# Optimization experiments

Measured on AMD Instinct MI355X. Metric: run time of the kernel, lower is better.

## Reference

```python
import jax, jax.numpy as jnp
import numpy as np

N_NODES = 25000
N_EDGES = 400000
IN = 128
HID = [64, 64, 128]
HEADS = [4, 4, 1]
SLOPE = 0.01  # F.leaky_relu default


def _xavier(key, shape):
    fan_out, fan_in = shape
    std = (2.0 / (fan_in + fan_out)) ** 0.5
    return std * jax.random.normal(key, shape, dtype=jnp.float32)


def setup_inputs() -> dict:
    key = jax.random.key(0)
    ks = jax.random.split(key, 24)
    inp = {}
    inp['x'] = jax.random.normal(ks[0], (N_NODES, IN), dtype=jnp.float32)
    inp['edge_weight'] = jax.random.uniform(ks[1], (N_EDGES,), dtype=jnp.float32)
    inp['edge_src'] = jax.random.randint(ks[2], (N_EDGES,), 0, N_NODES)
    inp['edge_dst'] = jax.random.randint(ks[3], (N_EDGES,), 0, N_NODES)
    inp['pos_src'] = jax.random.randint(ks[4], (100000,), 0, N_NODES)
    inp['pos_dst'] = jax.random.randint(ks[5], (100000,), 0, N_NODES)
    inp['neg_src'] = jax.random.randint(ks[6], (100000,), 0, N_NODES)
    inp['neg_dst'] = jax.random.randint(ks[7], (100000,), 0, N_NODES)
    # GAT layer params: fc weight [H*F, in], attn vector [F], bias [H*F]
    dims_in = [IN, HID[0] * HEADS[0], HID[1] * HEADS[1]]
    for l in range(3):
        H, F = HEADS[l], HID[l]
        inp[f'W{l}'] = _xavier(ks[8 + 2 * l], (H * F, dims_in[l]))
        inp[f'a{l}'] = _xavier(ks[9 + 2 * l], (1, F)).reshape(F)
        inp[f'b{l}'] = jnp.zeros((H * F,), dtype=jnp.float32)
    # predictor MLP: 128 -> 64 -> 32 -> 1 (Linear with bias)
    d = HID[2]
    inp['pW1'] = _xavier(ks[14], (d // 2, d)); inp['pb1'] = jnp.zeros((d // 2,), jnp.float32)
    inp['pW2'] = _xavier(ks[15], (d // 4, d // 2)); inp['pb2'] = jnp.zeros((d // 4,), jnp.float32)
    inp['pW3'] = _xavier(ks[16], (1, d // 4)); inp['pb3'] = jnp.zeros((1,), jnp.float32)
    return inp


def _leaky(x, slope=SLOPE):
    return jnp.where(x >= 0, x, slope * x)


def _gat_layer(x, W, a, b, src, dst, ew, H, F):
    N = x.shape[0]
    h = (x @ W.T).reshape(N, H, F)               # [N,H,F]
    hs = h[src]                                   # [E,H,F] gathered src feats
    # GATv2-style score: attn_fc(q_src + k_dst) per head
    score = jnp.einsum('ehf,f->eh', hs + h[dst], a)   # [E,H]
    e = _leaky(score + jnp.log1p(ew)[:, None])         # [E,H]
    # segment softmax over edges grouped by destination node
    m = jax.ops.segment_max(e, dst, num_segments=N)    # [N,H]
    m = jnp.where(jnp.isfinite(m), m, 0.0)             # guard empty segments
    ex = jnp.exp(e - m[dst])
    s = jax.ops.segment_sum(ex, dst, num_segments=N)   # [N,H]
    alpha = ex / jnp.maximum(s[dst], 1e-20)            # [E,H]
    out = jax.ops.segment_sum(alpha[:, :, None] * hs, dst, num_segments=N)  # [N,H,F]
    return out.reshape(N, H * F) + b


def _predictor(z, pW1, pb1, pW2, pb2, pW3, pb3):
    z = _leaky(z @ pW1.T + pb1, 0.2)
    z = _leaky(z @ pW2.T + pb2, 0.2)
    return z @ pW3.T + pb3


def reference(x, edge_weight, W0, a0, b0, W1, a1, b1, W2, a2, b2,
              pW1, pb1, pW2, pb2, pW3, pb3,
              edge_src, edge_dst, pos_src, pos_dst, neg_src, neg_dst):
    h = _gat_layer(x, W0, a0, b0, edge_src, edge_dst, edge_weight, HEADS[0], HID[0])
    h = _leaky(h)
    h = _gat_layer(h, W1, a1, b1, edge_src, edge_dst, edge_weight, HEADS[1], HID[1])
    h = _leaky(h)
    h = _gat_layer(h, W2, a2, b2, edge_src, edge_dst, edge_weight, HEADS[2], HID[2])
    gat_embedding = h
    h_pos = _predictor(h[pos_src] * h[pos_dst], pW1, pb1, pW2, pb2, pW3, pb3)
    h_neg = _predictor(h[neg_src] * h[neg_dst], pW1, pb1, pW2, pb2, pW3, pb3)
    return (h_pos, h_neg, gat_embedding)
```

## Files before the change

### kernel.cpp

```cpp
#include <hip/hip_runtime.h>
#include <math.h>

#define N_IN 128

__device__ __forceinline__ float leaky01(float x) { return x >= 0.f ? x : 0.01f * x; }
__device__ __forceinline__ float leaky02(float x) { return x >= 0.f ? x : 0.2f * x; }

__global__ void k_count(const int* __restrict__ edst, int* __restrict__ deg, int E) {
    int e = blockIdx.x * 256 + threadIdx.x;
    if (e < E) atomicAdd(&deg[edst[e]], 1);
}

__global__ void k_scan1(const int* __restrict__ deg, int* __restrict__ rowptr,
                        int* __restrict__ bsum, int n) {
    __shared__ int s[256];
    int b = blockIdx.x, t = threadIdx.x;
    int idx = b * 256 + t;
    int v = (idx < n) ? deg[idx] : 0;
    s[t] = v;
    __syncthreads();
    for (int off = 1; off < 256; off <<= 1) {
        int x = (t >= off) ? s[t - off] : 0;
        __syncthreads();
        s[t] += x;
        __syncthreads();
    }
    if (idx < n) rowptr[idx + 1] = s[t];
    if (t == 255) bsum[b] = s[255];
}

__global__ void k_scan2(const int* __restrict__ bsum, int* __restrict__ boff, int nb) {
    __shared__ int s[128];
    int t = threadIdx.x;
    int v = (t < nb) ? bsum[t] : 0;
    s[t] = v;
    __syncthreads();
    for (int off = 1; off < 128; off <<= 1) {
        int x = (t >= off) ? s[t - off] : 0;
        __syncthreads();
        s[t] += x;
        __syncthreads();
    }
    if (t < nb) boff[t] = s[t] - v;
}

__global__ void k_scan3(int* __restrict__ rowptr, const int* __restrict__ boff, int n) {
    int idx = blockIdx.x * 256 + threadIdx.x;
    if (idx < n) rowptr[idx + 1] += boff[idx >> 8];
    if (idx == 0) rowptr[0] = 0;
}

__global__ void k_fill(const int* __restrict__ esrc, const int* __restrict__ edst,
                       const float* __restrict__ ew, const int* __restrict__ rowptr,
                       int* __restrict__ cursor, int* __restrict__ eid,
                       int* __restrict__ csrc, float* __restrict__ clew, int E) {
    int e = blockIdx.x * 256 + threadIdx.x;
    if (e >= E) return;
    int d = edst[e];
    int slot = rowptr[d] + atomicAdd(&cursor[d], 1);
    eid[slot] = e;
    csrc[slot] = esrc[e];
    clew[slot] = log1pf(ew[e]);
}

__global__ void k_sortseg(const int* __restrict__ rowptr, int* __restrict__ eid,
                          int* __restrict__ csrc, float* __restrict__ clew, int n) {
    int v = blockIdx.x * 256 + threadIdx.x;
    if (v >= n) return;
    int b = rowptr[v], e = rowptr[v + 1];
    for (int i = b + 1; i < e; i++) {
        int ke = eid[i], ks = csrc[i];
        float kl = clew[i];
        int j = i - 1;
        while (j >= b && eid[j] > ke) {
            eid[j + 1] = eid[j]; csrc[j + 1] = csrc[j]; clew[j + 1] = clew[j];
            j--;
        }
        eid[j + 1] = ke; csrc[j + 1] = ks; clew[j + 1] = kl;
    }
}

__global__ __launch_bounds__(256) void k_gemm(const float* __restrict__ X,
                                              const float* __restrict__ W,
                                              float* __restrict__ C,
                                              int N, int K, int M,
                                              const float* __restrict__ avec,
                                              float* __restrict__ qaOut,
                                              int H, int F) {
    __shared__ float Xs[8][132];
    __shared__ float Ws[8][132];
    __shared__ float qred[128][17];
    int r0 = blockIdx.y * 128;
    int c0 = blockIdx.x * 128;
    int t = threadIdx.x;
    int ty = t >> 4, tx = t & 15;

    float acc[8][8];
#pragma unroll
    for (int i = 0; i < 8; i++)
#pragma unroll
        for (int j = 0; j < 8; j++) acc[i][j] = 0.f;

    int lr = t >> 1;
    int lk = (t & 1) * 4;
    bool xok = (r0 + lr) < N;
    const float* Xp = X + (size_t)(r0 + lr) * K + lk;
    const float* Wp = W + (size_t)(c0 + lr) * K + lk;

    for (int k0 = 0; k0 < K; k0 += 8) {
        float4 xv = xok ? *(const float4*)(Xp + k0) : make_float4(0.f, 0.f, 0.f, 0.f);
        float4 wv = *(const float4*)(Wp + k0);
        __syncthreads();
        Xs[lk + 0][lr] = xv.x; Xs[lk + 1][lr] = xv.y; Xs[lk + 2][lr] = xv.z; Xs[lk + 3][lr] = xv.w;
        Ws[lk + 0][lr] = wv.x; Ws[lk + 1][lr] = wv.y; Ws[lk + 2][lr] = wv.z; Ws[lk + 3][lr] = wv.w;
        __syncthreads();
#pragma unroll
        for (int k = 0; k < 8; k++) {
            float4 a0 = *(const float4*)&Xs[k][ty * 8];
            float4 a1 = *(const float4*)&Xs[k][ty * 8 + 4];
            float4 b0 = *(const float4*)&Ws[k][tx * 8];
            float4 b1 = *(const float4*)&Ws[k][tx * 8 + 4];
            float av[8] = {a0.x, a0.y, a0.z, a0.w, a1.x, a1.y, a1.z, a1.w};
            float bv[8] = {b0.x, b0.y, b0.z, b0.w, b1.x, b1.y, b1.z, b1.w};
#pragma unroll
            for (int i = 0; i < 8; i++)
#pragma unroll
                for (int j = 0; j < 8; j++) acc[i][j] += av[i] * bv[j];
        }
    }

#pragma unroll
    for (int i = 0; i < 8; i++) {
        int row = r0 + ty * 8 + i;
        if (row < N) {
            float4 v0 = make_float4(acc[i][0], acc[i][1], acc[i][2], acc[i][3]);
            float4 v1 = make_float4(acc[i][4], acc[i][5], acc[i][6], acc[i][7]);
            *(float4*)&C[(size_t)row * M + c0 + tx * 8] = v0;
            *(float4*)&C[(size_t)row * M + c0 + tx * 8 + 4] = v1;
        }
    }

    if (qaOut) {
        int f0 = (c0 + tx * 8) & (F - 1);
        float4 a0 = *(const float4*)&avec[f0];
        float4 a1 = *(const float4*)&avec[f0 + 4];
#pragma unroll
        for (int i = 0; i < 8; i++) {
            float s = acc[i][0] * a0.x + acc[i][1] * a0.y + acc[i][2] * a0.z + acc[i][3] * a0.w
                    + acc[i][4] * a1.x + acc[i][5] * a1.y + acc[i][6] * a1.z + acc[i][7] * a1.w;
            qred[ty * 8 + i][tx] = s;
        }
        __syncthreads();
        if (t < 128) {
            int R = r0 + t;
            if (R < N) {
                float s0 = 0.f, s1 = 0.f;
#pragma unroll
                for (int x = 0; x < 8; x++) { s0 += qred[t][x]; s1 += qred[t][x + 8]; }
                if (F == 64) {
                    int hb = c0 >> 6;
                    qaOut[(size_t)R * H + hb] = s0;
                    qaOut[(size_t)R * H + hb + 1] = s1;
                } else {
                    qaOut[R] = s0 + s1;
                }
            }
        }
    }
}

template <int H>
__global__ __launch_bounds__(256) void k_stats(const float* __restrict__ qa,
                                               const int* __restrict__ rowptr,
                                               const int* __restrict__ csr_src,
                                               const float* __restrict__ csr_lew,
                                               float* __restrict__ alf, int N) {
    int w = threadIdx.x >> 6;
    int l = threadIdx.x & 63;
    int n = blockIdx.x * 4 + w;
    if (n >= N) return;
    int beg = rowptr[n], end = rowptr[n + 1];
    if (beg >= end) return;

    float qd[H];
#pragma unroll
    for (int h = 0; h < H; h++) qd[h] = qa[(size_t)n * H + h];

    float mx[H];
#pragma unroll
    for (int h = 0; h < H; h++) mx[h] = -1e30f;
    for (int i = beg + l; i < end; i += 64) {
        int src = csr_src[i];
        float lw = csr_lew[i];
#pragma unroll
        for (int h = 0; h < H; h++) {
            float sc = leaky01(qa[(size_t)src * H + h] + qd[h] + lw);
            mx[h] = fmaxf(mx[h], sc);
        }
    }
#pragma unroll
    for (int h = 0; h < H; h++) {
        for (int off = 32; off > 0; off >>= 1)
            mx[h] = fmaxf(mx[h], __shfl_xor(mx[h], off, 64));
    }

    float sm[H];
#pragma unroll
    for (int h = 0; h < H; h++) sm[h] = 0.f;
    for (int i = beg + l; i < end; i += 64) {
        int src = csr_src[i];
        float lw = csr_lew[i];
#pragma unroll
        for (int h = 0; h < H; h++) {
            float sc = leaky01(qa[(size_t)src * H + h] + qd[h] + lw);
            sm[h] += __expf(sc - mx[h]);
        }
    }
#pragma unroll
    for (int h = 0; h < H; h++) {
        for (int off = 32; off > 0; off >>= 1)
            sm[h] += __shfl_xor(sm[h], off, 64);
    }
    float inv[H];
#pragma unroll
    for (int h = 0; h < H; h++) inv[h] = 1.f / fmaxf(sm[h], 1e-20f);

    for (int i = beg + l; i < end; i += 64) {
        int src = csr_src[i];
        float lw = csr_lew[i];
        float av[H];
#pragma unroll
        for (int h = 0; h < H; h++) {
            float sc = leaky01(qa[(size_t)src * H + h] + qd[h] + lw);
            av[h] = __expf(sc - mx[h]) * inv[h];
        }
        if (H == 4) {
            *(float4*)&alf[(size_t)i * 4] = make_float4(av[0], av[1], av[2], av[3]);
        } else {
            alf[i] = av[0];
        }
    }
}

template <int H, int F, int VW, bool LOUT>
__global__ __launch_bounds__(256) void k_aggv(const float* __restrict__ feat,
                                              const float* __restrict__ alf,
                                              const float* __restrict__ bias,
                                              const int* __restrict__ rowptr,
                                              const int* __restrict__ csr_src,
                                              float* __restrict__ out, int N) {
    constexpr int M = H * F;
    __shared__ int sh_src[4][64];
    __shared__ float sh_alpha[4][64 * H];
    int w = threadIdx.x >> 6, l = threadIdx.x & 63;
    int n = blockIdx.x * 4 + w;
    if (n >= N) return;
    int beg = rowptr[n];
    int deg = rowptr[n + 1] - beg;
    int c = l * VW;
    const int hh = c / F;

    float acc[VW];
#pragma unroll
    for (int j = 0; j < VW; j++) acc[j] = 0.f;

    for (int c0 = 0; c0 < deg; c0 += 64) {
        int cn = min(64, deg - c0);
        if (l < cn) {
            sh_src[w][l] = csr_src[beg + c0 + l];
            if (H == 4)
                *(float4*)&sh_alpha[w][l * 4] = *(const float4*)&alf[(size_t)(beg + c0 + l) * 4];
            else
                sh_alpha[w][l] = alf[beg + c0 + l];
        }
        int i = 0;
        for (; i + 2 <= cn; i += 2) {
            int s0 = sh_src[w][i], s1 = sh_src[w][i + 1];
            float a0 = sh_alpha[w][i * H + hh], a1 = sh_alpha[w][(i + 1) * H + hh];
            float f0[VW], f1[VW];
            if (VW == 4) {
                float4 v0 = *(const float4*)&feat[(size_t)s0 * M + c];
                float4 v1 = *(const float4*)&feat[(size_t)s1 * M + c];
                f0[0] = v0.x; f0[1] = v0.y; f0[2] = v0.z; f0[3] = v0.w;
                f1[0] = v1.x; f1[1] = v1.y; f1[2] = v1.z; f1[3] = v1.w;
            } else {
                float2 v0 = *(const float2*)&feat[(size_t)s0 * M + c];
                float2 v1 = *(const float2*)&feat[(size_t)s1 * M + c];
                f0[0] = v0.x; f0[1] = v0.y;
                f1[0] = v1.x; f1[1] = v1.y;
            }
#pragma unroll
            for (int j = 0; j < VW; j++) acc[j] += a0 * f0[j] + a1 * f1[j];
        }
        if (i < cn) {
            int s0 = sh_src[w][i];
            float a0 = sh_alpha[w][i * H + hh];
            float f0[VW];
            if (VW == 4) {
                float4 v0 = *(const float4*)&feat[(size_t)s0 * M + c];
                f0[0] = v0.x; f0[1] = v0.y; f0[2] = v0.z; f0[3] = v0.w;
            } else {
                float2 v0 = *(const float2*)&feat[(size_t)s0 * M + c];
                f0[0] = v0.x; f0[1] = v0.y;
            }
#pragma unroll
            for (int j = 0; j < VW; j++) acc[j] += a0 * f0[j];
        }
    }

#pragma unroll
    for (int j = 0; j < VW; j++) {
        float r = acc[j] + bias[c + j];
        if (LOUT) r = leaky01(r);
        out[(size_t)n * M + c + j] = r;
    }
}

__global__ __launch_bounds__(256) void k_predf6(const float* __restrict__ h2,
                                                const int* __restrict__ ps, const int* __restrict__ pd,
                                                const int* __restrict__ ns, const int* __restrict__ nd,
                                                const float* __restrict__ W1, const float* __restrict__ b1,
                                                const float* __restrict__ W2, const float* __restrict__ b2,
                                                const float* __restrict__ W3, const float* __restrict__ b3,
                                                float* __restrict__ out, int npos, int ntot) {
    __shared__ float Zs[128 * 36];
    __shared__ float Wc[32 * 68];
    __shared__ int sp[128], dp[128];

    int t = threadIdx.x;
    int p0 = blockIdx.x * 128;
    int ty2 = t >> 3;
    int tx2 = t & 7;

    if (t < 128) {
        int pr = p0 + t;
        int s = 0, d = 0;
        if (pr < ntot) {
            if (pr < npos) { s = ps[pr]; d = pd[pr]; }
            else           { s = ns[pr - npos]; d = nd[pr - npos]; }
        }
        sp[t] = s; dp[t] = d;
    }
    __syncthreads();

    float acc[4][8];
#pragma unroll
    for (int i = 0; i < 4; i++)
#pragma unroll
        for (int j = 0; j < 8; j++) acc[i][j] = 0.f;

    int sr = t >> 3;
    int sq = t & 7;

    for (int kc = 0; kc < 128; kc += 32) {
#pragma unroll
        for (int it = 0; it < 4; ++it) {
            int r = it * 32 + sr;
            int s = sp[r], d = dp[r];
            float4 a = *(const float4*)&h2[(size_t)s * 128 + kc + sq * 4];
            float4 b = *(const float4*)&h2[(size_t)d * 128 + kc + sq * 4];
            *(float4*)&Zs[r * 36 + sq * 4] =
                make_float4(a.x * b.x, a.y * b.y, a.z * b.z, a.w * b.w);
        }
        {
            int out_ = t & 63;
            int kh = (t >> 6) * 8;
            const float* wr = W1 + (size_t)out_ * 128 + kc + kh;
#pragma unroll
            for (int c = 0; c < 2; c++) {
                float4 wv = *(const float4*)(wr + c * 4);
                Wc[(kh + c * 4 + 0) * 68 + out_] = wv.x;
                Wc[(kh + c * 4 + 1) * 68 + out_] = wv.y;
                Wc[(kh + c * 4 + 2) * 68 + out_] = wv.z;
                Wc[(kh + c * 4 + 3) * 68 + out_] = wv.w;
            }
        }
        __syncthreads();
#pragma unroll
        for (int k4 = 0; k4 < 8; ++k4) {
            float4 a4[4];
#pragma unroll
            for (int i = 0; i < 4; i++)
                a4[i] = *(const float4*)&Zs[(ty2 + 32 * i) * 36 + k4 * 4];
#pragma unroll
            for (int kk = 0; kk < 4; ++kk) {
                float4 bA = *(const float4*)&Wc[(k4 * 4 + kk) * 68 + tx2 * 8];
                float4 bB = *(const float4*)&Wc[(k4 * 4 + kk) * 68 + tx2 * 8 + 4];
                float bv[8] = {bA.x, bA.y, bA.z, bA.w, bB.x, bB.y, bB.z, bB.w};
#pragma unroll
                for (int i = 0; i < 4; i++) {
                    float a = (kk == 0) ? a4[i].x : (kk == 1) ? a4[i].y : (kk == 2) ? a4[i].z : a4[i].w;
#pragma unroll
                    for (int j = 0; j < 8; j++) acc[i][j] += a * bv[j];
                }
            }
        }
        __syncthreads();
    }

    {
        float4 b1a = *(const float4*)&b1[tx2 * 8];
        float4 b1b = *(const float4*)&b1[tx2 * 8 + 4];
        float bb[8] = {b1a.x, b1a.y, b1a.z, b1a.w, b1b.x, b1b.y, b1b.z, b1b.w};
#pragma unroll
        for (int i = 0; i < 4; i++)
#pragma unroll
            for (int j = 0; j < 8; j++) acc[i][j] += bb[j];
    }

    float t2[32];
#pragma unroll
    for (int o = 0; o < 32; o++) t2[o] = b2[o];

    if (tx2 < 4) {
#pragma unroll
        for (int i = 0; i < 4; i++) {
            int row = ty2 + 32 * i;
            *(float4*)&Zs[row * 36 + tx2 * 8] =
                make_float4(acc[i][0], acc[i][1], acc[i][2], acc[i][3]);
            *(float4*)&Zs[row * 36 + tx2 * 8 + 4] =
                make_float4(acc[i][4], acc[i][5], acc[i][6], acc[i][7]);
        }
    }
    __syncthreads();
    if (t < 128) {
        for (int j = 0; j < 32; j += 4) {
            float4 v4 = *(const float4*)&Zs[t * 36 + j];
            float v0 = leaky02(v4.x), v1 = leaky02(v4.y), v2 = leaky02(v4.z), v3 = leaky02(v4.w);
#pragma unroll
            for (int o = 0; o < 32; o++) {
                const float* w2 = W2 + (size_t)o * 64 + j;
                t2[o] += v0 * w2[0] + v1 * w2[1] + v2 * w2[2] + v3 * w2[3];
            }
        }
    }
    __syncthreads();
    if (tx2 >= 4) {
#pragma unroll
        for (int i = 0; i < 4; i++) {
            int row = ty2 + 32 * i;
            *(float4*)&Zs[row * 36 + (tx2 - 4) * 8] =
                make_float4(acc[i][0], acc[i][1], acc[i][2], acc[i][3]);
            *(float4*)&Zs[row * 36 + (tx2 - 4) * 8 + 4] =
                make_float4(acc[i][4], acc[i][5], acc[i][6], acc[i][7]);
        }
    }
    __syncthreads();
    if (t < 128) {
        for (int j = 0; j < 32; j += 4) {
            float4 v4 = *(const float4*)&Zs[t * 36 + j];
            float v0 = leaky02(v4.x), v1 = leaky02(v4.y), v2 = leaky02(v4.z), v3 = leaky02(v4.w);
#pragma unroll
            for (int o = 0; o < 32; o++) {
                const float* w2 = W2 + (size_t)o * 64 + 32 + j;
                t2[o] += v0 * w2[0] + v1 * w2[1] + v2 * w2[2] + v3 * w2[3];
            }
        }
        float o3 = b3[0];
#pragma unroll
        for (int o = 0; o < 32; o++) o3 += leaky02(t2[o]) * W3[o];
        if (p0 + t < ntot) out[p0 + t] = o3;
    }
}

extern "C" void kernel_launch(void* const* d_in, const int* in_sizes, int n_in,
                              void* d_out, int out_size, void* d_ws, size_t ws_size,
                              hipStream_t stream) {
    const float* x    = (const float*)d_in[0];
    const float* ew   = (const float*)d_in[1];
    const int* esrc   = (const int*)d_in[2];
    const int* edst   = (const int*)d_in[3];
    const int* pos_s  = (const int*)d_in[4];
    const int* pos_d  = (const int*)d_in[5];
    const int* neg_s  = (const int*)d_in[6];
    const int* neg_d  = (const int*)d_in[7];
    const float* W0 = (const float*)d_in[8];
    const float* a0 = (const float*)d_in[9];
    const float* b0 = (const float*)d_in[10];
    const float* W1 = (const float*)d_in[11];
    const float* a1 = (const float*)d_in[12];
    const float* b1 = (const float*)d_in[13];
    const float* W2 = (const float*)d_in[14];
    const float* a2 = (const float*)d_in[15];
    const float* b2 = (const float*)d_in[16];
    const float* pW1 = (const float*)d_in[17];
    const float* pb1 = (const float*)d_in[18];
    const float* pW2 = (const float*)d_in[19];
    const float* pb2 = (const float*)d_in[20];
    const float* pW3 = (const float*)d_in[21];
    const float* pb3 = (const float*)d_in[22];

    const int N = in_sizes[0] / N_IN;
    const int E = in_sizes[1];
    const int NP = in_sizes[4];

    size_t off = 0;
    auto alloc = [&](size_t bytes) {
        void* p = (char*)d_ws + off;
        off += (bytes + 255) & ~(size_t)255;
        return p;
    };
    int* deg      = (int*)alloc((size_t)N * 4);
    int* cursor   = (int*)alloc((size_t)N * 4);
    int* rowptr   = (int*)alloc((size_t)(N + 1) * 4);
    int* bsum     = (int*)alloc(512);
    int* boff     = (int*)alloc(512);
    int* csr_eid  = (int*)alloc((size_t)E * 4);
    int* csr_src  = (int*)alloc((size_t)E * 4);
    float* csr_lew = (float*)alloc((size_t)E * 4);
    float* qa     = (float*)alloc((size_t)N * 4 * 4);
    float* alf    = (float*)alloc((size_t)E * 4 * 4);
    float* A      = (float*)alloc((size_t)N * 256 * 4);
    float* B      = (float*)alloc((size_t)N * 256 * 4);
    (void)ws_size; (void)n_in; (void)out_size;

    float* out_pred = (float*)d_out;
    float* emb      = (float*)d_out + 2 * NP;

    hipMemsetAsync(deg, 0, (size_t)N * 4, stream);
    hipMemsetAsync(cursor, 0, (size_t)N * 4, stream);

    int eb = (E + 255) / 256;
    int nb = (N + 255) / 256;
    k_count<<<eb, 256, 0, stream>>>(edst, deg, E);
    k_scan1<<<nb, 256, 0, stream>>>(deg, rowptr, bsum, N);
    k_scan2<<<1, 128, 0, stream>>>(bsum, boff, nb);
    k_scan3<<<nb, 256, 0, stream>>>(rowptr, boff, N);
    k_fill<<<eb, 256, 0, stream>>>(esrc, edst, ew, rowptr, cursor, csr_eid, csr_src, csr_lew, E);
    k_sortseg<<<(N + 255) / 256, 256, 0, stream>>>(rowptr, csr_eid, csr_src, csr_lew, N);

    int rb = (N + 127) / 128;
    int sb = (N + 3) / 4;

    k_gemm<<<dim3(2, rb), 256, 0, stream>>>(x, W0, A, N, 128, 256, a0, qa, 4, 64);
    k_stats<4><<<sb, 256, 0, stream>>>(qa, rowptr, csr_src, csr_lew, alf, N);
    k_aggv<4, 64, 4, true><<<sb, 256, 0, stream>>>(A, alf, b0, rowptr, csr_src, B, N);

    k_gemm<<<dim3(2, rb), 256, 0, stream>>>(B, W1, A, N, 256, 256, a1, qa, 4, 64);
    k_stats<4><<<sb, 256, 0, stream>>>(qa, rowptr, csr_src, csr_lew, alf, N);
    k_aggv<4, 64, 4, true><<<sb, 256, 0, stream>>>(A, alf, b1, rowptr, csr_src, B, N);

    k_gemm<<<dim3(1, rb), 256, 0, stream>>>(B, W2, A, N, 256, 128, a2, qa, 1, 128);
    k_stats<1><<<sb, 256, 0, stream>>>(qa, rowptr, csr_src, csr_lew, alf, N);
    k_aggv<1, 128, 2, false><<<sb, 256, 0, stream>>>(A, alf, b2, rowptr, csr_src, emb, N);

    int ntot = 2 * NP;
    k_predf6<<<(ntot + 127) / 128, 256, 0, stream>>>(emb, pos_s, pos_d, neg_s, neg_d,
                                                     pW1, pb1, pW2, pb2, pW3, pb3,
                                                     out_pred, NP, ntot);
}
```

Measured before the change: 529.9 us.

## Bucket predictor pairs by source node and remap blocks per XCD for locality

Adds a counting sort (count, scan, fill) that groups the 200k predictor pairs by source-node bucket of 128 and builds a permutation. The predictor kernel reads pairs through that permutation and scatters its results back to their original positions. Block indices are also remapped so that consecutive buckets land on the same XCD, which is meant to improve L2 reuse of the source rows of h2. This adds three small kernels, two memsets and an extra indirection, and the destination rows are still gathered at random.

```diff
diff --git a/kernel.cpp b/kernel.cpp
--- a/kernel.cpp
+++ b/kernel.cpp
@@ -78,6 +78,40 @@
         }
         eid[j + 1] = ke; csrc[j + 1] = ks; clew[j + 1] = kl;
     }
+}
+
+__global__ void k_bcount(const int* __restrict__ ps, const int* __restrict__ ns,
+                         int* __restrict__ bcnt, int npos, int ntot) {
+    int p = blockIdx.x * 256 + threadIdx.x;
+    if (p >= ntot) return;
+    int s = (p < npos) ? ps[p] : ns[p - npos];
+    atomicAdd(&bcnt[s >> 7], 1);
+}
+
+__global__ void k_bscan(const int* __restrict__ bcnt, int* __restrict__ bbase, int nb) {
+    __shared__ int s[256];
+    int t = threadIdx.x;
+    int v = (t < nb) ? bcnt[t] : 0;
+    s[t] = v;
+    __syncthreads();
+    for (int off = 1; off < 256; off <<= 1) {
+        int x = (t >= off) ? s[t - off] : 0;
+        __syncthreads();
+        s[t] += x;
+        __syncthreads();
+    }
+    if (t < nb) bbase[t] = s[t] - v;
+}
+
+__global__ void k_bfill(const int* __restrict__ ps, const int* __restrict__ ns,
+                        const int* __restrict__ bbase, int* __restrict__ bcur,
+                        int* __restrict__ perm, int npos, int ntot) {
+    int p = blockIdx.x * 256 + threadIdx.x;
+    if (p >= ntot) return;
+    int s = (p < npos) ? ps[p] : ns[p - npos];
+    int b = s >> 7;
+    int slot = bbase[b] + atomicAdd(&bcur[b], 1);
+    perm[slot] = p;
 }
 
 __global__ __launch_bounds__(256) void k_gemm(const float* __restrict__ X,
@@ -316,30 +350,38 @@
     }
 }
 
-__global__ __launch_bounds__(256) void k_predf6(const float* __restrict__ h2,
+__global__ __launch_bounds__(256) void k_predf7(const float* __restrict__ h2,
                                                 const int* __restrict__ ps, const int* __restrict__ pd,
                                                 const int* __restrict__ ns, const int* __restrict__ nd,
+                                                const int* __restrict__ perm,
                                                 const float* __restrict__ W1, const float* __restrict__ b1,
                                                 const float* __restrict__ W2, const float* __restrict__ b2,
                                                 const float* __restrict__ W3, const float* __restrict__ b3,
                                                 float* __restrict__ out, int npos, int ntot) {
     __shared__ float Zs[128 * 36];
     __shared__ float Wc[32 * 68];
-    __shared__ int sp[128], dp[128];
+    __shared__ int sp[128], dp[128], pidx[128];
 
     int t = threadIdx.x;
-    int p0 = blockIdx.x * 128;
+    int G = gridDim.x;
+    int b = blockIdx.x;
+    int xcd = b & 7;
+    int q = G >> 3, r = G & 7;
+    int v = (xcd < r ? xcd * (q + 1) : r * (q + 1) + (xcd - r) * q) + (b >> 3);
+    int p0 = v * 128;
+
     int ty2 = t >> 3;
     int tx2 = t & 7;
 
     if (t < 128) {
         int pr = p0 + t;
-        int s = 0, d = 0;
+        int s = 0, d = 0, pe = -1;
         if (pr < ntot) {
-            if (pr < npos) { s = ps[pr]; d = pd[pr]; }
-            else           { s = ns[pr - npos]; d = nd[pr - npos]; }
-        }
-        sp[t] = s; dp[t] = d;
+            pe = perm[pr];
+            if (pe < npos) { s = ps[pe]; d = pd[pe]; }
+            else           { s = ns[pe - npos]; d = nd[pe - npos]; }
+        }
+        sp[t] = s; dp[t] = d; pidx[t] = pe;
     }
     __syncthreads();
 
@@ -355,12 +397,12 @@
     for (int kc = 0; kc < 128; kc += 32) {
 #pragma unroll
         for (int it = 0; it < 4; ++it) {
-            int r = it * 32 + sr;
-            int s = sp[r], d = dp[r];
+            int rr = it * 32 + sr;
+            int s = sp[rr], d = dp[rr];
             float4 a = *(const float4*)&h2[(size_t)s * 128 + kc + sq * 4];
-            float4 b = *(const float4*)&h2[(size_t)d * 128 + kc + sq * 4];
-            *(float4*)&Zs[r * 36 + sq * 4] =
-                make_float4(a.x * b.x, a.y * b.y, a.z * b.z, a.w * b.w);
+            float4 bb = *(const float4*)&h2[(size_t)d * 128 + kc + sq * 4];
+            *(float4*)&Zs[rr * 36 + sq * 4] =
+                make_float4(a.x * bb.x, a.y * bb.y, a.z * bb.z, a.w * bb.w);
         }
         {
             int out_ = t & 63;
@@ -459,7 +501,8 @@
         float o3 = b3[0];
 #pragma unroll
         for (int o = 0; o < 32; o++) o3 += leaky02(t2[o]) * W3[o];
-        if (p0 + t < ntot) out[p0 + t] = o3;
+        int pe = pidx[t];
+        if (pe >= 0) out[pe] = o3;
     }
 }
 
@@ -512,6 +555,10 @@
     float* alf    = (float*)alloc((size_t)E * 4 * 4);
     float* A      = (float*)alloc((size_t)N * 256 * 4);
     float* B      = (float*)alloc((size_t)N * 256 * 4);
+    int* bcnt     = (int*)alloc(1024);
+    int* bbase    = (int*)alloc(1024);
+    int* bcur     = (int*)alloc(1024);
+    int* perm     = (int*)alloc((size_t)2 * NP * 4);
     (void)ws_size; (void)n_in; (void)out_size;
 
     float* out_pred = (float*)d_out;
@@ -519,6 +566,8 @@
 
     hipMemsetAsync(deg, 0, (size_t)N * 4, stream);
     hipMemsetAsync(cursor, 0, (size_t)N * 4, stream);
+    hipMemsetAsync(bcnt, 0, 1024, stream);
+    hipMemsetAsync(bcur, 0, 1024, stream);
 
     int eb = (E + 255) / 256;
     int nb = (N + 255) / 256;
@@ -529,6 +578,13 @@
     k_fill<<<eb, 256, 0, stream>>>(esrc, edst, ew, rowptr, cursor, csr_eid, csr_src, csr_lew, E);
     k_sortseg<<<(N + 255) / 256, 256, 0, stream>>>(rowptr, csr_eid, csr_src, csr_lew, N);
 
+    int ntot = 2 * NP;
+    int pb = (ntot + 255) / 256;
+    int NB = (N + 127) / 128;
+    k_bcount<<<pb, 256, 0, stream>>>(pos_s, neg_s, bcnt, NP, ntot);
+    k_bscan<<<1, 256, 0, stream>>>(bcnt, bbase, NB);
+    k_bfill<<<pb, 256, 0, stream>>>(pos_s, neg_s, bbase, bcur, perm, NP, ntot);
+
     int rb = (N + 127) / 128;
     int sb = (N + 3) / 4;
 
@@ -544,8 +600,7 @@
     k_stats<1><<<sb, 256, 0, stream>>>(qa, rowptr, csr_src, csr_lew, alf, N);
     k_aggv<1, 128, 2, false><<<sb, 256, 0, stream>>>(A, alf, b2, rowptr, csr_src, emb, N);
 
-    int ntot = 2 * NP;
-    k_predf6<<<(ntot + 127) / 128, 256, 0, stream>>>(emb, pos_s, pos_d, neg_s, neg_d,
+    k_predf7<<<(ntot + 127) / 128, 256, 0, stream>>>(emb, pos_s, pos_d, neg_s, neg_d, perm,
                                                      pW1, pb1, pW2, pb2, pW3, pb3,
                                                      out_pred, NP, ntot);
 }
```

Result: slower. 764.3 us (+44.2%).

## Fuse edge softmax stats into aggregation kernel, caching scores in LDS

Applied to the files above, without the earlier changes.

Merges the per-destination softmax kernel (max, sum, alpha write) into the aggregation kernel. Scores for nodes with degree up to 128 are kept in shared memory, so the three passes over edges and the per-edge alpha buffer round trip through global memory go away. High-degree nodes fall back to recomputing scores from global memory. This removes three launches and the E*H alpha writes and reads, at the cost of more shared memory per block and more work per wave in one kernel.

```diff
diff --git a/kernel.cpp b/kernel.cpp
--- a/kernel.cpp
+++ b/kernel.cpp
@@ -169,89 +169,18 @@
     }
 }
 
-template <int H>
-__global__ __launch_bounds__(256) void k_stats(const float* __restrict__ qa,
-                                               const int* __restrict__ rowptr,
-                                               const int* __restrict__ csr_src,
-                                               const float* __restrict__ csr_lew,
-                                               float* __restrict__ alf, int N) {
-    int w = threadIdx.x >> 6;
-    int l = threadIdx.x & 63;
-    int n = blockIdx.x * 4 + w;
-    if (n >= N) return;
-    int beg = rowptr[n], end = rowptr[n + 1];
-    if (beg >= end) return;
-
-    float qd[H];
-#pragma unroll
-    for (int h = 0; h < H; h++) qd[h] = qa[(size_t)n * H + h];
-
-    float mx[H];
-#pragma unroll
-    for (int h = 0; h < H; h++) mx[h] = -1e30f;
-    for (int i = beg + l; i < end; i += 64) {
-        int src = csr_src[i];
-        float lw = csr_lew[i];
-#pragma unroll
-        for (int h = 0; h < H; h++) {
-            float sc = leaky01(qa[(size_t)src * H + h] + qd[h] + lw);
-            mx[h] = fmaxf(mx[h], sc);
-        }
-    }
-#pragma unroll
-    for (int h = 0; h < H; h++) {
-        for (int off = 32; off > 0; off >>= 1)
-            mx[h] = fmaxf(mx[h], __shfl_xor(mx[h], off, 64));
-    }
-
-    float sm[H];
-#pragma unroll
-    for (int h = 0; h < H; h++) sm[h] = 0.f;
-    for (int i = beg + l; i < end; i += 64) {
-        int src = csr_src[i];
-        float lw = csr_lew[i];
-#pragma unroll
-        for (int h = 0; h < H; h++) {
-            float sc = leaky01(qa[(size_t)src * H + h] + qd[h] + lw);
-            sm[h] += __expf(sc - mx[h]);
-        }
-    }
-#pragma unroll
-    for (int h = 0; h < H; h++) {
-        for (int off = 32; off > 0; off >>= 1)
-            sm[h] += __shfl_xor(sm[h], off, 64);
-    }
-    float inv[H];
-#pragma unroll
-    for (int h = 0; h < H; h++) inv[h] = 1.f / fmaxf(sm[h], 1e-20f);
-
-    for (int i = beg + l; i < end; i += 64) {
-        int src = csr_src[i];
-        float lw = csr_lew[i];
-        float av[H];
-#pragma unroll
-        for (int h = 0; h < H; h++) {
-            float sc = leaky01(qa[(size_t)src * H + h] + qd[h] + lw);
-            av[h] = __expf(sc - mx[h]) * inv[h];
-        }
-        if (H == 4) {
-            *(float4*)&alf[(size_t)i * 4] = make_float4(av[0], av[1], av[2], av[3]);
-        } else {
-            alf[i] = av[0];
-        }
-    }
-}
-
 template <int H, int F, int VW, bool LOUT>
-__global__ __launch_bounds__(256) void k_aggv(const float* __restrict__ feat,
-                                              const float* __restrict__ alf,
+__global__ __launch_bounds__(256) void k_fagg(const float* __restrict__ feat,
+                                              const float* __restrict__ qa,
                                               const float* __restrict__ bias,
                                               const int* __restrict__ rowptr,
                                               const int* __restrict__ csr_src,
+                                              const float* __restrict__ csr_lew,
                                               float* __restrict__ out, int N) {
     constexpr int M = H * F;
-    __shared__ int sh_src[4][64];
-    __shared__ float sh_alpha[4][64 * H];
+    constexpr int CACHE = 128;
+    __shared__ int sh_src[4][CACHE];
+    __shared__ float sh_sc[4][CACHE * H];
     int w = threadIdx.x >> 6, l = threadIdx.x & 63;
     int n = blockIdx.x * 4 + w;
     if (n >= N) return;
@@ -264,47 +193,144 @@
 #pragma unroll
     for (int j = 0; j < VW; j++) acc[j] = 0.f;
 
-    for (int c0 = 0; c0 < deg; c0 += 64) {
-        int cn = min(64, deg - c0);
-        if (l < cn) {
-            sh_src[w][l] = csr_src[beg + c0 + l];
-            if (H == 4)
-                *(float4*)&sh_alpha[w][l * 4] = *(const float4*)&alf[(size_t)(beg + c0 + l) * 4];
-            else
-                sh_alpha[w][l] = alf[beg + c0 + l];
-        }
-        int i = 0;
-        for (; i + 2 <= cn; i += 2) {
-            int s0 = sh_src[w][i], s1 = sh_src[w][i + 1];
-            float a0 = sh_alpha[w][i * H + hh], a1 = sh_alpha[w][(i + 1) * H + hh];
-            float f0[VW], f1[VW];
-            if (VW == 4) {
-                float4 v0 = *(const float4*)&feat[(size_t)s0 * M + c];
-                float4 v1 = *(const float4*)&feat[(size_t)s1 * M + c];
-                f0[0] = v0.x; f0[1] = v0.y; f0[2] = v0.z; f0[3] = v0.w;
-                f1[0] = v1.x; f1[1] = v1.y; f1[2] = v1.z; f1[3] = v1.w;
-            } else {
-                float2 v0 = *(const float2*)&feat[(size_t)s0 * M + c];
-                float2 v1 = *(const float2*)&feat[(size_t)s1 * M + c];
-                f0[0] = v0.x; f0[1] = v0.y;
-                f1[0] = v1.x; f1[1] = v1.y;
-            }
-#pragma unroll
-            for (int j = 0; j < VW; j++) acc[j] += a0 * f0[j] + a1 * f1[j];
-        }
-        if (i < cn) {
-            int s0 = sh_src[w][i];
-            float a0 = sh_alpha[w][i * H + hh];
-            float f0[VW];
-            if (VW == 4) {
-                float4 v0 = *(const float4*)&feat[(size_t)s0 * M + c];
-                f0[0] = v0.x; f0[1] = v0.y; f0[2] = v0.z; f0[3] = v0.w;
-            } else {
-                float2 v0 = *(const float2*)&feat[(size_t)s0 * M + c];
-                f0[0] = v0.x; f0[1] = v0.y;
-            }
-#pragma unroll
-            for (int j = 0; j < VW; j++) acc[j] += a0 * f0[j];
+    if (deg > 0) {
+        float qd[H];
+#pragma unroll
+        for (int h = 0; h < H; h++) qd[h] = qa[(size_t)n * H + h];
+
+        if (deg <= CACHE) {
+            float mx[H];
+#pragma unroll
+            for (int h = 0; h < H; h++) mx[h] = -1e30f;
+            for (int i = l; i < deg; i += 64) {
+                int src = csr_src[beg + i];
+                float lw = csr_lew[beg + i];
+                sh_src[w][i] = src;
+#pragma unroll
+                for (int h = 0; h < H; h++) {
+                    float sc = leaky01(qa[(size_t)src * H + h] + qd[h] + lw);
+                    sh_sc[w][i * H + h] = sc;
+                    mx[h] = fmaxf(mx[h], sc);
+                }
+            }
+#pragma unroll
+            for (int h = 0; h < H; h++) {
+                for (int off = 32; off > 0; off >>= 1)
+                    mx[h] = fmaxf(mx[h], __shfl_xor(mx[h], off, 64));
+            }
+            float sm[H];
+#pragma unroll
+            for (int h = 0; h < H; h++) sm[h] = 0.f;
+            for (int i = l; i < deg; i += 64) {
+#pragma unroll
+                for (int h = 0; h < H; h++) sm[h] += __expf(sh_sc[w][i * H + h] - mx[h]);
+            }
+#pragma unroll
+            for (int h = 0; h < H; h++) {
+                for (int off = 32; off > 0; off >>= 1)
+                    sm[h] += __shfl_xor(sm[h], off, 64);
+            }
+            float inv[H];
+#pragma unroll
+            for (int h = 0; h < H; h++) inv[h] = 1.f / fmaxf(sm[h], 1e-20f);
+            for (int i = l; i < deg; i += 64) {
+#pragma unroll
+                for (int h = 0; h < H; h++)
+                    sh_sc[w][i * H + h] = __expf(sh_sc[w][i * H + h] - mx[h]) * inv[h];
+            }
+            int i = 0;
+            for (; i + 2 <= deg; i += 2) {
+                int s0 = sh_src[w][i], s1 = sh_src[w][i + 1];
+                float a0 = sh_sc[w][i * H + hh], a1 = sh_sc[w][(i + 1) * H + hh];
+                float f0[VW], f1[VW];
+                if (VW == 4) {
+                    float4 v0 = *(const float4*)&feat[(size_t)s0 * M + c];
+                    float4 v1 = *(const float4*)&feat[(size_t)s1 * M + c];
+                    f0[0] = v0.x; f0[1] = v0.y; f0[2] = v0.z; f0[3] = v0.w;
+                    f1[0] = v1.x; f1[1] = v1.y; f1[2] = v1.z; f1[3] = v1.w;
+                } else {
+                    float2 v0 = *(const float2*)&feat[(size_t)s0 * M + c];
+                    float2 v1 = *(const float2*)&feat[(size_t)s1 * M + c];
+                    f0[0] = v0.x; f0[1] = v0.y;
+                    f1[0] = v1.x; f1[1] = v1.y;
+                }
+#pragma unroll
+                for (int j = 0; j < VW; j++) acc[j] += a0 * f0[j] + a1 * f1[j];
+            }
+            if (i < deg) {
+                int s0 = sh_src[w][i];
+                float a0 = sh_sc[w][i * H + hh];
+                float f0[VW];
+                if (VW == 4) {
+                    float4 v0 = *(const float4*)&feat[(size_t)s0 * M + c];
+                    f0[0] = v0.x; f0[1] = v0.y; f0[2] = v0.z; f0[3] = v0.w;
+                } else {
+                    float2 v0 = *(const float2*)&feat[(size_t)s0 * M + c];
+                    f0[0] = v0.x; f0[1] = v0.y;
+                }
+#pragma unroll
+                for (int j = 0; j < VW; j++) acc[j] += a0 * f0[j];
+            }
+        } else {
+            int end = beg + deg;
+            float mx[H];
+#pragma unroll
+            for (int h = 0; h < H; h++) mx[h] = -1e30f;
+            for (int i = beg + l; i < end; i += 64) {
+                int src = csr_src[i];
+                float lw = csr_lew[i];
+#pragma unroll
+                for (int h = 0; h < H; h++)
+                    mx[h] = fmaxf(mx[h], leaky01(qa[(size_t)src * H + h] + qd[h] + lw));
+            }
+#pragma unroll
+            for (int h = 0; h < H; h++) {
+                for (int off = 32; off > 0; off >>= 1)
+                    mx[h] = fmaxf(mx[h], __shfl_xor(mx[h], off, 64));
+            }
+            float sm[H];
+#pragma unroll
+            for (int h = 0; h < H; h++) sm[h] = 0.f;
+            for (int i = beg + l; i < end; i += 64) {
+                int src = csr_src[i];
+                float lw = csr_lew[i];
+#pragma unroll
+                for (int h = 0; h < H; h++)
+                    sm[h] += __expf(leaky01(qa[(size_t)src * H + h] + qd[h] + lw) - mx[h]);
+            }
+#pragma unroll
+            for (int h = 0; h < H; h++) {
+                for (int off = 32; off > 0; off >>= 1)
+                    sm[h] += __shfl_xor(sm[h], off, 64);
+            }
+            float inv[H];
+#pragma unroll
+            for (int h = 0; h < H; h++) inv[h] = 1.f / fmaxf(sm[h], 1e-20f);
+
+            for (int c0 = 0; c0 < deg; c0 += 64) {
+                int cn = min(64, deg - c0);
+                if (l < cn) {
+                    int src = csr_src[beg + c0 + l];
+                    float lw = csr_lew[beg + c0 + l];
+                    sh_src[w][l] = src;
+#pragma unroll
+                    for (int h = 0; h < H; h++)
+                        sh_sc[w][l * H + h] =
+                            __expf(leaky01(qa[(size_t)src * H + h] + qd[h] + lw) - mx[h]) * inv[h];
+                }
+                for (int i = 0; i < cn; i++) {
+                    int s0 = sh_src[w][i];
+                    float a0 = sh_sc[w][i * H + hh];
+                    if (VW == 4) {
+                        float4 v0 = *(const float4*)&feat[(size_t)s0 * M + c];
+                        acc[0] += a0 * v0.x; acc[1] += a0 * v0.y;
+                        acc[2] += a0 * v0.z; acc[3] += a0 * v0.w;
+                    } else {
+                        float2 v0 = *(const float2*)&feat[(size_t)s0 * M + c];
+                        acc[0] += a0 * v0.x; acc[1] += a0 * v0.y;
+                    }
+                }
+            }
         }
     }
 
@@ -509,7 +535,6 @@
     int* csr_src  = (int*)alloc((size_t)E * 4);
     float* csr_lew = (float*)alloc((size_t)E * 4);
     float* qa     = (float*)alloc((size_t)N * 4 * 4);
-    float* alf    = (float*)alloc((size_t)E * 4 * 4);
     float* A      = (float*)alloc((size_t)N * 256 * 4);
     float* B      = (float*)alloc((size_t)N * 256 * 4);
     (void)ws_size; (void)n_in; (void)out_size;
@@ -533,16 +558,13 @@
     int sb = (N + 3) / 4;
 
     k_gemm<<<dim3(2, rb), 256, 0, stream>>>(x, W0, A, N, 128, 256, a0, qa, 4, 64);
-    k_stats<4><<<sb, 256, 0, stream>>>(qa, rowptr, csr_src, csr_lew, alf, N);
-    k_aggv<4, 64, 4, true><<<sb, 256, 0, stream>>>(A, alf, b0, rowptr, csr_src, B, N);
+    k_fagg<4, 64, 4, true><<<sb, 256, 0, stream>>>(A, qa, b0, rowptr, csr_src, csr_lew, B, N);
 
     k_gemm<<<dim3(2, rb), 256, 0, stream>>>(B, W1, A, N, 256, 256, a1, qa, 4, 64);
-    k_stats<4><<<sb, 256, 0, stream>>>(qa, rowptr, csr_src, csr_lew, alf, N);
-    k_aggv<4, 64, 4, true><<<sb, 256, 0, stream>>>(A, alf, b1, rowptr, csr_src, B, N);
+    k_fagg<4, 64, 4, true><<<sb, 256, 0, stream>>>(A, qa, b1, rowptr, csr_src, csr_lew, B, N);
 
     k_gemm<<<dim3(1, rb), 256, 0, stream>>>(B, W2, A, N, 256, 128, a2, qa, 1, 128);
-    k_stats<1><<<sb, 256, 0, stream>>>(qa, rowptr, csr_src, csr_lew, alf, N);
-    k_aggv<1, 128, 2, false><<<sb, 256, 0, stream>>>(A, alf, b2, rowptr, csr_src, emb, N);
+    k_fagg<1, 128, 2, false><<<sb, 256, 0, stream>>>(A, qa, b2, rowptr, csr_src, csr_lew, emb, N);
 
     int ntot = 2 * NP;
     k_predf6<<<(ntot + 127) / 128, 256, 0, stream>>>(emb, pos_s, pos_d, neg_s, neg_d,
```

Measured after the change: 499.9 us. -5.7%, faster.
